# Kernel optimization log

Measured on AMD Instinct MI355X. Metric: run time of the kernel, lower is better.

Reference implementation:

```python
import jax, jax.numpy as jnp
import numpy as np

EPS = 1e-5

def activation_quant(x):
    # per-token absmax int8 quant: scale = 127 / max|x| along last dim
    scale = 127.0 / jnp.clip(jnp.max(jnp.abs(x), axis=-1, keepdims=True), EPS)
    return jnp.clip(jnp.round(x * scale), -128, 127) / scale

def weight_quant(w):
    # per-tensor ternary quant: scale = 1 / mean|w|, values in {-1,0,1}/scale
    scale = 1.0 / jnp.clip(jnp.mean(jnp.abs(w)), EPS)
    return jnp.clip(jnp.round(w * scale), -1, 1) / scale

def setup_inputs() -> dict:
    key = jax.random.key(0)
    kx, kw = jax.random.split(key)
    x = jax.random.normal(kx, (4, 2048, 4096), dtype=jnp.float32)
    weight = jax.random.normal(kw, (16384, 4096), dtype=jnp.float32) * 0.02
    return {"x": x, "weight": weight}

def reference(x, weight):
    # straight-through estimator: forward uses quantized values
    x_q = x + jax.lax.stop_gradient(activation_quant(x) - x)
    w_q = weight + jax.lax.stop_gradient(weight_quant(weight) - weight)
    # y = x_q @ w_q.T  (F.linear), out: [B, S, out_features]
    return jnp.einsum('bsi,oi->bso', x_q, w_q)
```

## Files before the change

kernel.cpp:

```cpp
#include <hip/hip_runtime.h>
#include <stdint.h>


typedef int v4i __attribute__((ext_vector_type(4)));

#define QEPS 1e-5f

#define M_DIM 8192
#define N_DIM 16384
#define K_DIM 4096

#define BM 128
#define BN 128
#define BK 64

__global__ void wabs_sum(const float* __restrict__ w, double* __restrict__ acc,
                         int n4) {
    int idx = blockIdx.x * blockDim.x + threadIdx.x;
    int stride = gridDim.x * blockDim.x;
    const float4* w4 = (const float4*)w;
    double s = 0.0;
    for (int i = idx; i < n4; i += stride) {
        float4 v = w4[i];
        s += (double)(fabsf(v.x) + fabsf(v.y) + fabsf(v.z) + fabsf(v.w));
    }
    #pragma unroll
    for (int off = 32; off > 0; off >>= 1)
        s += __shfl_down(s, off, 64);
    __shared__ double sm[4];
    int lane = threadIdx.x & 63, wv = threadIdx.x >> 6;
    if (lane == 0) sm[wv] = s;
    __syncthreads();
    if (threadIdx.x == 0) {
        atomicAdd(acc, sm[0] + sm[1] + sm[2] + sm[3]);
    }
}

__device__ __forceinline__ int tq1(float v, float s) {
    float q = rintf(v * s);
    q = fminf(fmaxf(q, -1.0f), 1.0f);
    return (int)q;
}

__global__ void wquant(const float* __restrict__ w, int8_t* __restrict__ tw,
                       const double* __restrict__ acc, double inv_cnt, int n4) {
    double mean = (*acc) * inv_cnt;
    float mclip = (float)fmax(mean, (double)QEPS);
    float sw = 1.0f / mclip;
    int idx = blockIdx.x * blockDim.x + threadIdx.x;
    int stride = gridDim.x * blockDim.x;
    const float4* w4 = (const float4*)w;
    uint32_t* out = (uint32_t*)tw;
    for (int i = idx; i < n4; i += stride) {
        float4 v = w4[i];
        uint32_t a = (uint32_t)(tq1(v.x, sw) & 0xff);
        uint32_t b = (uint32_t)(tq1(v.y, sw) & 0xff);
        uint32_t c = (uint32_t)(tq1(v.z, sw) & 0xff);
        uint32_t d = (uint32_t)(tq1(v.w, sw) & 0xff);
        out[i] = a | (b << 8) | (c << 16) | (d << 24);
    }
}

__device__ __forceinline__ int q8(float v, float s) {
    float q = rintf(v * s);
    q = fminf(fmaxf(q, -128.0f), 127.0f);
    return (int)q;
}

__global__ void xquant(const float* __restrict__ x, int8_t* __restrict__ qx,
                       float* __restrict__ rowscale) {
    int row = blockIdx.x;
    int t = threadIdx.x;
    const float4* xr = (const float4*)(x + (size_t)row * K_DIM);
    float4 v[4];
    float m = 0.0f;
    #pragma unroll
    for (int i = 0; i < 4; i++) {
        v[i] = xr[t + i * 256];
        m = fmaxf(m, fmaxf(fmaxf(fabsf(v[i].x), fabsf(v[i].y)),
                           fmaxf(fabsf(v[i].z), fabsf(v[i].w))));
    }
    #pragma unroll
    for (int off = 32; off > 0; off >>= 1)
        m = fmaxf(m, __shfl_down(m, off, 64));
    __shared__ float sm[4];
    int lane = t & 63, wv = t >> 6;
    if (lane == 0) sm[wv] = m;
    __syncthreads();
    m = fmaxf(fmaxf(sm[0], sm[1]), fmaxf(sm[2], sm[3]));
    float mc = fmaxf(m, QEPS);
    float scale = 127.0f / mc;
    if (t == 0) rowscale[row] = mc * (1.0f / 127.0f);
    uint32_t* qr = (uint32_t*)(qx + (size_t)row * K_DIM);
    #pragma unroll
    for (int i = 0; i < 4; i++) {
        uint32_t a = (uint32_t)(q8(v[i].x, scale) & 0xff);
        uint32_t b = (uint32_t)(q8(v[i].y, scale) & 0xff);
        uint32_t c = (uint32_t)(q8(v[i].z, scale) & 0xff);
        uint32_t d = (uint32_t)(q8(v[i].w, scale) & 0xff);
        qr[t + i * 256] = a | (b << 8) | (c << 16) | (d << 24);
    }
}

__device__ __forceinline__ void async_copy16(const void* g, void* l) {
    __builtin_amdgcn_global_load_lds(
        (__attribute__((address_space(1))) void*)g,
        (__attribute__((address_space(3))) void*)l, 16, 0, 0);
}

__global__ __launch_bounds__(256, 2)
void gemm_i8(const int8_t* __restrict__ A,
             const int8_t* __restrict__ B,
             const float* __restrict__ rowscale,
             const double* __restrict__ macc, double inv_cnt,
             float* __restrict__ C) {
    __shared__ int8_t As[BM * BK];
    __shared__ int8_t Bs[BN * BK];

    const int tid = threadIdx.x;
    const int wave = tid >> 6;
    const int lane = tid & 63;
    const int bm = blockIdx.y * BM;
    const int bn = blockIdx.x * BN;
    const int wm = (wave & 1) << 6;
    const int wn = (wave >> 1) << 6;

    v4i acc[4][4] = {};

    const int cbase = wave * 64 + lane;
    const int8_t* Abase = A + (size_t)bm * K_DIM;
    const int8_t* Bbase = B + (size_t)bn * K_DIM;

    const int fr = lane & 15;
    const int kq = (lane >> 4) * 16;

    for (int kt = 0; kt < K_DIM / BK; kt++) {
        const int k0 = kt * BK;
        __syncthreads();
        #pragma unroll
        for (int i = 0; i < 2; i++) {
            int c = cbase + i * 256;
            int row = c >> 2, koff = (c & 3) * 16;
            async_copy16(Abase + (size_t)row * K_DIM + k0 + koff,
                         As + i * 4096 + wave * 1024);
        }
        #pragma unroll
        for (int i = 0; i < 2; i++) {
            int c = cbase + i * 256;
            int row = c >> 2, koff = (c & 3) * 16;
            async_copy16(Bbase + (size_t)row * K_DIM + k0 + koff,
                         Bs + i * 4096 + wave * 1024);
        }
        __syncthreads();

        v4i a[4], b[4];
        #pragma unroll
        for (int mi = 0; mi < 4; mi++)
            a[mi] = *(const v4i*)(As + (wm + mi * 16 + fr) * BK + kq);
        #pragma unroll
        for (int ni = 0; ni < 4; ni++)
            b[ni] = *(const v4i*)(Bs + (wn + ni * 16 + fr) * BK + kq);
        #pragma unroll
        for (int mi = 0; mi < 4; mi++) {
            #pragma unroll
            for (int ni = 0; ni < 4; ni++) {
                acc[mi][ni] = __builtin_amdgcn_mfma_i32_16x16x64_i8(
                    a[mi], b[ni], acc[mi][ni], 0, 0, 0);
            }
        }
    }

    float mw = (float)fmax((*macc) * inv_cnt, (double)QEPS);
    const int col0 = bn + wn + (lane & 15);
    const int rbase = bm + wm + (lane >> 4) * 4;
    #pragma unroll
    for (int mi = 0; mi < 4; mi++) {
        #pragma unroll
        for (int r = 0; r < 4; r++) {
            int row = rbase + mi * 16 + r;
            float rs = rowscale[row] * mw;
            float* crow = C + (size_t)row * N_DIM;
            #pragma unroll
            for (int ni = 0; ni < 4; ni++) {
                crow[col0 + ni * 16] = (float)acc[mi][ni][r] * rs;
            }
        }
    }
}

extern "C" void kernel_launch(void* const* d_in, const int* in_sizes, int n_in,
                              void* d_out, int out_size, void* d_ws,
                              size_t ws_size, hipStream_t stream) {
    const float* x = (const float*)d_in[0];
    const float* w = (const float*)d_in[1];
    float* out = (float*)d_out;

    const size_t QX_BYTES = (size_t)M_DIM * K_DIM;
    const size_t TW_BYTES = (size_t)N_DIM * K_DIM;
    int8_t* qx = (int8_t*)d_ws;
    int8_t* tw = (int8_t*)d_ws + QX_BYTES;
    float* rowscale = (float*)((char*)d_ws + QX_BYTES + TW_BYTES);
    double* macc = (double*)((char*)d_ws + QX_BYTES + TW_BYTES +
                             (size_t)M_DIM * sizeof(float));

    const double inv_cnt = 1.0 / (double)((size_t)N_DIM * K_DIM);

    hipMemsetAsync(macc, 0, sizeof(double), stream);
    wabs_sum<<<1024, 256, 0, stream>>>(w, macc, (N_DIM * K_DIM) / 4);
    wquant<<<2048, 256, 0, stream>>>(w, tw, macc, inv_cnt, (N_DIM * K_DIM) / 4);
    xquant<<<M_DIM, 256, 0, stream>>>(x, qx, rowscale);
    dim3 grid(N_DIM / BN, M_DIM / BM);
    gemm_i8<<<grid, 256, 0, stream>>>(qx, tw, rowscale, macc, inv_cnt, out);
}
```

Baseline: 1.381 ms.

## Rewrite int8 GEMM with 256x256 tiles, 4-stage async LDS pipeline and swizzle

The int8 MFMA GEMM moves to 256x256 block tiles with 8 waves, so each wave computes a 128x64 sub-tile. K tiles stream through a 4-slot LDS ring, with global-to-LDS loads issued several stages ahead and waited on with explicit vmcnt counts and barriers. The LDS layout is XOR-swizzled to avoid bank conflicts, MFMA sections run at raised wave priority, and block indices are remapped across XCDs for L2 locality. The aim is to hide global load latency and raise MFMA utilization. In exchange it uses much more LDS (128KB) and more registers, and it relies on hand-counted waitcnt values being correct.

```diff
diff --git a/kernel.cpp b/kernel.cpp
--- a/kernel.cpp
+++ b/kernel.cpp
@@ -9,10 +9,6 @@
 #define M_DIM 8192
 #define N_DIM 16384
 #define K_DIM 4096
-
-#define BM 128
-#define BN 128
-#define BK 64
 
 __global__ void wabs_sum(const float* __restrict__ w, double* __restrict__ acc,
                          int n4) {
@@ -102,83 +98,133 @@
     }
 }
 
+
+#define BM 256
+#define BN 256
+#define KT 64
+#define SLOT 16384
+
 __device__ __forceinline__ void async_copy16(const void* g, void* l) {
     __builtin_amdgcn_global_load_lds(
         (__attribute__((address_space(1))) void*)g,
         (__attribute__((address_space(3))) void*)l, 16, 0, 0);
 }
 
-__global__ __launch_bounds__(256, 2)
+#define WAITVM_IMM(N) asm volatile("s_waitcnt vmcnt(" #N ")" ::: "memory")
+#define WAITVM(N) WAITVM_IMM(N)
+
+__global__ __launch_bounds__(512, 2)
 void gemm_i8(const int8_t* __restrict__ A,
              const int8_t* __restrict__ B,
              const float* __restrict__ rowscale,
              const double* __restrict__ macc, double inv_cnt,
              float* __restrict__ C) {
-    __shared__ int8_t As[BM * BK];
-    __shared__ int8_t Bs[BN * BK];
+    __shared__ int8_t As[4][SLOT];
+    __shared__ int8_t Bs[4][SLOT];
 
     const int tid = threadIdx.x;
     const int wave = tid >> 6;
     const int lane = tid & 63;
-    const int bm = blockIdx.y * BM;
-    const int bn = blockIdx.x * BN;
-    const int wm = (wave & 1) << 6;
-    const int wn = (wave >> 1) << 6;
-
-    v4i acc[4][4] = {};
-
-    const int cbase = wave * 64 + lane;
-    const int8_t* Abase = A + (size_t)bm * K_DIM;
-    const int8_t* Bbase = B + (size_t)bn * K_DIM;
-
+
+    const int orig = blockIdx.x;
+    const int idx = (orig & 7) * 256 + (orig >> 3);
+    const int bm = (idx >> 6) * BM;
+    const int bn = (idx & 63) * BN;
+
+    const int wr = wave >> 2;
+    const int wc = wave & 3;
     const int fr = lane & 15;
-    const int kq = (lane >> 4) * 16;
-
-    for (int kt = 0; kt < K_DIM / BK; kt++) {
-        const int k0 = kt * BK;
-        __syncthreads();
-        #pragma unroll
-        for (int i = 0; i < 2; i++) {
-            int c = cbase + i * 256;
-            int row = c >> 2, koff = (c & 3) * 16;
-            async_copy16(Abase + (size_t)row * K_DIM + k0 + koff,
-                         As + i * 4096 + wave * 1024);
-        }
-        #pragma unroll
-        for (int i = 0; i < 2; i++) {
-            int c = cbase + i * 256;
-            int row = c >> 2, koff = (c & 3) * 16;
-            async_copy16(Bbase + (size_t)row * K_DIM + k0 + koff,
-                         Bs + i * 4096 + wave * 1024);
-        }
-        __syncthreads();
-
-        v4i a[4], b[4];
-        #pragma unroll
-        for (int mi = 0; mi < 4; mi++)
-            a[mi] = *(const v4i*)(As + (wm + mi * 16 + fr) * BK + kq);
-        #pragma unroll
-        for (int ni = 0; ni < 4; ni++)
-            b[ni] = *(const v4i*)(Bs + (wn + ni * 16 + fr) * BK + kq);
-        #pragma unroll
-        for (int mi = 0; mi < 4; mi++) {
-            #pragma unroll
-            for (int ni = 0; ni < 4; ni++) {
-                acc[mi][ni] = __builtin_amdgcn_mfma_i32_16x16x64_i8(
-                    a[mi], b[ni], acc[mi][ni], 0, 0, 0);
-            }
-        }
-    }
+    const int q  = lane >> 4;
+
+    const int sl   = (q ^ ((fr >> 1) & 3)) << 4;
+    const int aoff = (wr * 128 + fr) * 64 + sl;
+    const int boff = (wc * 64 + fr) * 64 + sl;
+
+    const int l2   = lane >> 2;
+    const int gcol = ((lane & 3) ^ ((lane >> 3) & 3)) << 4;
+    const int c0   = wave;
+    const int c1   = 8 + wave;
+    const int8_t* aS0 = A + (size_t)(bm + c0 * 16 + l2) * K_DIM + gcol;
+    const int8_t* aS1 = A + (size_t)(bm + c1 * 16 + l2) * K_DIM + gcol;
+    const int8_t* bS0 = B + (size_t)(bn + c0 * 16 + l2) * K_DIM + gcol;
+    const int8_t* bS1 = B + (size_t)(bn + c1 * 16 + l2) * K_DIM + gcol;
+
+    v4i acc[8][4] = {};
+    v4i a[8];
+
+#define STAGE_A(T) do { const int _s = (T) & 3; const int _k = (T) * KT;    \
+        async_copy16(aS0 + _k, &As[_s][c0 * 1024]);                         \
+        async_copy16(aS1 + _k, &As[_s][c1 * 1024]); } while (0)
+#define STAGE_B(T) do { const int _s = (T) & 3; const int _k = (T) * KT;    \
+        async_copy16(bS0 + _k, &Bs[_s][c0 * 1024]);                         \
+        async_copy16(bS1 + _k, &Bs[_s][c1 * 1024]); } while (0)
+
+#define PHASE_A(T, DOSTAGE) do {                                            \
+        const int8_t* _as = As[(T) & 3];                                    \
+        const int8_t* _bs = Bs[(T) & 3];                                    \
+        v4i b0 = *(const v4i*)(_bs + boff);                                 \
+        v4i b1 = *(const v4i*)(_bs + boff + 1024);                          \
+        _Pragma("unroll")                                                   \
+        for (int mi = 0; mi < 8; mi++)                                      \
+            a[mi] = *(const v4i*)(_as + aoff + mi * 1024);                  \
+        if (DOSTAGE) STAGE_B((T) + 3);                                      \
+        __builtin_amdgcn_s_setprio(1);                                      \
+        _Pragma("unroll")                                                   \
+        for (int mi = 0; mi < 8; mi++)                                      \
+            acc[mi][0] = __builtin_amdgcn_mfma_i32_16x16x64_i8(             \
+                a[mi], b0, acc[mi][0], 0, 0, 0);                            \
+        _Pragma("unroll")                                                   \
+        for (int mi = 0; mi < 8; mi++)                                      \
+            acc[mi][1] = __builtin_amdgcn_mfma_i32_16x16x64_i8(             \
+                a[mi], b1, acc[mi][1], 0, 0, 0);                            \
+        __builtin_amdgcn_s_setprio(0);                                      \
+        __builtin_amdgcn_s_barrier();                                       \
+    } while (0)
+
+#define PHASE_B(T, DOSTAGE, VM) do {                                        \
+        const int8_t* _bs = Bs[(T) & 3];                                    \
+        v4i b2 = *(const v4i*)(_bs + boff + 2048);                          \
+        v4i b3 = *(const v4i*)(_bs + boff + 3072);                          \
+        if (DOSTAGE) STAGE_A((T) + 4);                                      \
+        __builtin_amdgcn_s_setprio(1);                                      \
+        _Pragma("unroll")                                                   \
+        for (int mi = 0; mi < 8; mi++)                                      \
+            acc[mi][2] = __builtin_amdgcn_mfma_i32_16x16x64_i8(             \
+                a[mi], b2, acc[mi][2], 0, 0, 0);                            \
+        _Pragma("unroll")                                                   \
+        for (int mi = 0; mi < 8; mi++)                                      \
+            acc[mi][3] = __builtin_amdgcn_mfma_i32_16x16x64_i8(             \
+                a[mi], b3, acc[mi][3], 0, 0, 0);                            \
+        __builtin_amdgcn_s_setprio(0);                                      \
+        WAITVM(VM);                                                         \
+        __builtin_amdgcn_s_barrier();                                       \
+    } while (0)
+
+    STAGE_A(0); STAGE_B(0); STAGE_A(1); STAGE_B(1);
+    STAGE_A(2); STAGE_B(2); STAGE_A(3);
+    WAITVM(10);
+    __builtin_amdgcn_s_barrier();
+
+    for (int t4 = 0; t4 < 60; t4 += 4) {
+        PHASE_A(t4 + 0, 1); PHASE_B(t4 + 0, 1, 10);
+        PHASE_A(t4 + 1, 1); PHASE_B(t4 + 1, 1, 10);
+        PHASE_A(t4 + 2, 1); PHASE_B(t4 + 2, 1, 10);
+        PHASE_A(t4 + 3, 1); PHASE_B(t4 + 3, 1, 10);
+    }
+    PHASE_A(60, 1); PHASE_B(60, 0, 8);
+    PHASE_A(61, 0); PHASE_B(61, 0, 4);
+    PHASE_A(62, 0); PHASE_B(62, 0, 0);
+    PHASE_A(63, 0); PHASE_B(63, 0, 63);
 
     float mw = (float)fmax((*macc) * inv_cnt, (double)QEPS);
-    const int col0 = bn + wn + (lane & 15);
-    const int rbase = bm + wm + (lane >> 4) * 4;
-    #pragma unroll
-    for (int mi = 0; mi < 4; mi++) {
+    const int col0 = bn + wc * 64 + fr;
+    const int rb   = bm + wr * 128 + q * 4;
+    #pragma unroll
+    for (int mi = 0; mi < 8; mi++) {
         #pragma unroll
         for (int r = 0; r < 4; r++) {
-            int row = rbase + mi * 16 + r;
-            float rs = rowscale[row] * mw;
+            const int row = rb + mi * 16 + r;
+            const float rs = rowscale[row] * mw;
             float* crow = C + (size_t)row * N_DIM;
             #pragma unroll
             for (int ni = 0; ni < 4; ni++) {
@@ -205,10 +251,9 @@
 
     const double inv_cnt = 1.0 / (double)((size_t)N_DIM * K_DIM);
 
-    hipMemsetAsync(macc, 0, sizeof(double), stream);
+    (void)hipMemsetAsync(macc, 0, sizeof(double), stream);
     wabs_sum<<<1024, 256, 0, stream>>>(w, macc, (N_DIM * K_DIM) / 4);
     wquant<<<2048, 256, 0, stream>>>(w, tw, macc, inv_cnt, (N_DIM * K_DIM) / 4);
     xquant<<<M_DIM, 256, 0, stream>>>(x, qx, rowscale);
-    dim3 grid(N_DIM / BN, M_DIM / BM);
-    gemm_i8<<<grid, 256, 0, stream>>>(qx, tw, rowscale, macc, inv_cnt, out);
-}
+    gemm_i8<<<2048, 512, 0, stream>>>(qx, tw, rowscale, macc, inv_cnt, out);
+}
```

New measurement: 1.324 ms. 1.04x faster.
